# Kernel optimization log

Hardware: AMD Instinct MI355X
Metric: run time of the kernel (lower is better)

The kernel has to match this reference:

```python
import jax, jax.numpy as jnp
import numpy as np

EMBED_DIM = 2048
N_HEADS = 16
HEAD_DIM = EMBED_DIM // N_HEADS  # 128
ROPE_BASE = 10000.0


def _rope(x):
    # x: (B, H, L, d) -- torchtune-style interleaved RoPE over position axis L
    L, d = x.shape[-2], x.shape[-1]
    inv_freq = 1.0 / (ROPE_BASE ** (jnp.arange(0, d, 2, dtype=jnp.float32) / d))  # (d/2,)
    freqs = jnp.arange(L, dtype=jnp.float32)[:, None] * inv_freq[None, :]          # (L, d/2)
    cos = jnp.cos(freqs).astype(x.dtype)
    sin = jnp.sin(freqs).astype(x.dtype)
    x1 = x[..., 0::2]  # (B,H,L,d/2)
    x2 = x[..., 1::2]
    out_even = x1 * cos - x2 * sin
    out_odd = x2 * cos + x1 * sin
    return jnp.stack([out_even, out_odd], axis=-1).reshape(x.shape)


def setup_inputs() -> dict:
    key = jax.random.key(0)
    ks = jax.random.split(key, 9)
    B, L, D = 64, 256, EMBED_DIM
    x = jax.random.normal(ks[0], (B, L, D), dtype=jnp.float32)
    s = 0.02
    wq = jax.random.normal(ks[1], (D, D), dtype=jnp.float32) * s
    wk = jax.random.normal(ks[2], (D, D), dtype=jnp.float32) * s
    wv = jax.random.normal(ks[3], (D, D), dtype=jnp.float32) * s
    wo = jax.random.normal(ks[4], (D, D), dtype=jnp.float32) * s
    bq = jax.random.normal(ks[5], (D,), dtype=jnp.float32) * s
    bk = jax.random.normal(ks[6], (D,), dtype=jnp.float32) * s
    bv = jax.random.normal(ks[7], (D,), dtype=jnp.float32) * s
    bo = jax.random.normal(ks[8], (D,), dtype=jnp.float32) * s
    return {"x": x, "wq": wq, "bq": bq, "wk": wk, "bk": bk,
            "wv": wv, "bv": bv, "wo": wo, "bo": bo}


def reference(x, wq, bq, wk, bk, wv, bv, wo, bo):
    B, L, D = x.shape
    H, hd = N_HEADS, HEAD_DIM

    def proj(w, b):
        y = jnp.einsum('bld,de->ble', x, w) + b
        return y.reshape(B, L, H, hd).transpose(0, 2, 1, 3)  # (B,H,L,hd)

    q = _rope(proj(wq, bq))
    k = _rope(proj(wk, bk))
    v = proj(wv, bv)

    scale = 1.0 / jnp.sqrt(jnp.asarray(hd, dtype=x.dtype))
    scores = jnp.einsum('bhqd,bhkd->bhqk', q, k) * scale  # (B,H,L,L)
    causal = jnp.tril(jnp.ones((L, L), dtype=bool))
    scores = jnp.where(causal[None, None], scores, -jnp.inf)
    attn = jax.nn.softmax(scores, axis=-1)
    out = jnp.einsum('bhqk,bhkd->bhqd', attn, v)  # (B,H,L,hd)
    out = out.transpose(0, 2, 1, 3).reshape(B, L, D)
    return jnp.einsum('bld,de->ble', out, wo) + bo
```

## Files before the change

### kernel.cpp

```cpp
#include <hip/hip_runtime.h>
#include <math.h>

typedef __bf16 bf16;
typedef float f32x4 __attribute__((ext_vector_type(4)));
typedef bf16  bf16x4 __attribute__((ext_vector_type(4)));
typedef bf16  bf16x8 __attribute__((ext_vector_type(8)));

#define N_B  64
#define N_L  256
#define N_H  16
#define N_D  2048
#define N_HD 128
#define M_TOT (N_B * N_L)

static __device__ __forceinline__ float bfbits_lo(unsigned u) {
  union { unsigned u; float f; } c; c.u = u << 16; return c.f;
}
static __device__ __forceinline__ float bfbits_hi(unsigned u) {
  union { unsigned u; float f; } c; c.u = u & 0xffff0000u; return c.f;
}

static __device__ __forceinline__ f32x4 shflx4(f32x4 v, int m) {
  f32x4 r;
  r[0] = __shfl_xor(v[0], m);
  r[1] = __shfl_xor(v[1], m);
  r[2] = __shfl_xor(v[2], m);
  r[3] = __shfl_xor(v[3], m);
  return r;
}
static __device__ __forceinline__ f32x4 max4(f32x4 a, f32x4 b) {
  f32x4 r;
  r[0] = fmaxf(a[0], b[0]); r[1] = fmaxf(a[1], b[1]);
  r[2] = fmaxf(a[2], b[2]); r[3] = fmaxf(a[3], b[3]);
  return r;
}

__global__ void k_cast_x(const float* __restrict__ x, bf16* __restrict__ xb, int n4) {
  int i = blockIdx.x * blockDim.x + threadIdx.x;
  int st = gridDim.x * blockDim.x;
  for (; i < n4; i += st) {
    float4 v = ((const float4*)x)[i];
    bf16x4 o;
    o[0] = (bf16)v.x; o[1] = (bf16)v.y; o[2] = (bf16)v.z; o[3] = (bf16)v.w;
    ((bf16x4*)xb)[i] = o;
  }
}

__global__ void k_transpose_w(const float* __restrict__ w, bf16* __restrict__ wt) {
  __shared__ float t[32][33];
  int n0 = blockIdx.x * 32, k0 = blockIdx.y * 32;
  t[threadIdx.y][threadIdx.x] = w[(size_t)(k0 + threadIdx.y) * N_D + n0 + threadIdx.x];
  __syncthreads();
  wt[(size_t)(n0 + threadIdx.y) * N_D + k0 + threadIdx.x] = (bf16)t[threadIdx.x][threadIdx.y];
}

__global__ void k_trig(float2* __restrict__ tab) {
  int idx = blockIdx.x * blockDim.x + threadIdx.x;
  if (idx < N_L * (N_HD / 2)) {
    int l = idx >> 6, i = idx & 63;
    float ang = (float)l * powf(10000.0f, -(float)(2 * i) / 128.0f);
    tab[idx].x = cosf(ang);
    tab[idx].y = sinf(ang);
  }
}


#define GLOAD(GP, LP) __builtin_amdgcn_global_load_lds( \
    (const __attribute__((address_space(1))) void*)(GP), \
    (__attribute__((address_space(3))) void*)(LP), 16, 0, 0)
#define BARR()  __builtin_amdgcn_s_barrier()
#define SCHED() __builtin_amdgcn_sched_barrier(0)
#define PRIO1() __builtin_amdgcn_s_setprio(1)
#define PRIO0() __builtin_amdgcn_s_setprio(0)
#define WAITLGKM() asm volatile("s_waitcnt lgkmcnt(0)" ::: "memory")
#define WAITVM4()  asm volatile("s_waitcnt vmcnt(4)" ::: "memory")

#define STAGE_A(X, KT, BUF) do { \
  GLOAD(Ag + (size_t)srcOffA[0][X] + (size_t)((KT) & 31) * 64, (BUF) + ldsOffA[0][X]); \
  GLOAD(Ag + (size_t)srcOffA[1][X] + (size_t)((KT) & 31) * 64, (BUF) + ldsOffA[1][X]); \
} while (0)
#define STAGE_B(X, KT, BUF) do { \
  GLOAD(Bg + (size_t)srcOffB[0][X] + (size_t)((KT) & 31) * 64, (BUF) + ldsOffB[0][X]); \
  GLOAD(Bg + (size_t)srcOffB[1][X] + (size_t)((KT) & 31) * 64, (BUF) + ldsOffB[1][X]); \
} while (0)

#define LDA(QM, BUF) do { \
  _Pragma("unroll") for (int i_ = 0; i_ < 4; ++i_) { \
    const int R_ = wm * 128 + ((QM) * 4 + i_) * 16 + lr; \
    _Pragma("unroll") for (int kk_ = 0; kk_ < 2; ++kk_) \
      afr[i_][kk_] = *(const bf16x8*)&(BUF)[R_ * 64 + (((kk_ * 4 + lg) ^ (R_ & 7)) << 3)]; \
  } \
} while (0)
#define LDB(DST, QN, BUF) do { \
  _Pragma("unroll") for (int j_ = 0; j_ < 2; ++j_) { \
    const int R_ = wn * 64 + ((QN) * 2 + j_) * 16 + lr; \
    _Pragma("unroll") for (int kk_ = 0; kk_ < 2; ++kk_) \
      DST[j_][kk_] = *(const bf16x8*)&(BUF)[R_ * 64 + (((kk_ * 4 + lg) ^ (R_ & 7)) << 3)]; \
  } \
} while (0)

#define MFMA16(BF, QM, QN) do { \
  _Pragma("unroll") for (int i_ = 0; i_ < 4; ++i_) \
  _Pragma("unroll") for (int j_ = 0; j_ < 2; ++j_) \
  _Pragma("unroll") for (int kk_ = 0; kk_ < 2; ++kk_) \
    acc[(QM) * 4 + i_][(QN) * 2 + j_] = __builtin_amdgcn_mfma_f32_16x16x32_bf16( \
        afr[i_][kk_], BF[j_][kk_], acc[(QM) * 4 + i_][(QN) * 2 + j_], 0, 0, 0); \
} while (0)

#define TILE(T, CURA, CURB, OTHA, OTHB) do { \
   \
  LDA(0, CURA); LDB(bfr0, 0, CURB); STAGE_B(1, (T) + 1, OTHB); \
  SCHED(); BARR(); WAITLGKM(); SCHED(); \
  PRIO1(); MFMA16(bfr0, 0, 0); PRIO0(); \
  SCHED(); BARR(); SCHED(); \
   \
  LDB(bfr1, 1, CURB); STAGE_A(1, (T) + 1, OTHA); \
  SCHED(); BARR(); WAITLGKM(); SCHED(); \
  PRIO1(); MFMA16(bfr1, 0, 1); PRIO0(); \
  SCHED(); BARR(); SCHED(); \
   \
  LDA(1, CURA); STAGE_A(0, (T) + 2, CURA); \
  SCHED(); BARR(); WAITLGKM(); SCHED(); \
  PRIO1(); MFMA16(bfr0, 1, 0); PRIO0(); \
  SCHED(); BARR(); SCHED(); \
   \
  STAGE_B(0, (T) + 2, CURB); \
  SCHED(); BARR(); SCHED(); \
  PRIO1(); MFMA16(bfr1, 1, 1); PRIO0(); \
  SCHED(); WAITVM4(); BARR(); SCHED(); \
} while (0)

template<int MODE>
__global__ __launch_bounds__(512, 2) void k_gemm256(
    const bf16* __restrict__ A, const bf16* __restrict__ BT,
    const float* __restrict__ bias, void* __restrict__ dstv,
    const float2* __restrict__ tab)
{
  __shared__ bf16 lds[2][2][256 * 64];
  const int bid = blockIdx.x;
  const int xcd = bid & 7, idx = bid >> 3;
  const int bm = xcd * 8 + (idx >> 3), bn = idx & 7;
  const int m0 = bm * 256, n0 = bn * 256;
  const int tid = threadIdx.x;
  const int wave = tid >> 6, lane = tid & 63;
  const int wm = wave >> 2, wn = wave & 3;
  const int lr = lane & 15, lg = lane >> 4;
  const bf16* __restrict__ Ag = A;
  const bf16* __restrict__ Bg = BT;

  int srcOffA[2][2], srcOffB[2][2], ldsOffA[2][2], ldsOffB[2][2];
  {
    const int g7 = tid & 7;
#pragma unroll
    for (int u = 0; u < 2; ++u) {
      const int rl  = u * 64 + (tid >> 3);
      const int rl0 = u * 64 + wave * 8;
#pragma unroll
      for (int X = 0; X < 2; ++X) {
        const int rA  = ((rl >> 6) << 7)  | (X << 6) | (rl & 63);
        const int rA0 = ((rl0 >> 6) << 7) | (X << 6) | (rl0 & 63);
        srcOffA[u][X] = (m0 + rA) * N_D + ((g7 ^ (rA & 7)) << 3);
        ldsOffA[u][X] = rA0 * 64;
        const int rB  = ((rl >> 5) << 6)  | (X << 5) | (rl & 31);
        const int rB0 = ((rl0 >> 5) << 6) | (X << 5) | (rl0 & 31);
        srcOffB[u][X] = (n0 + rB) * N_D + ((g7 ^ (rB & 7)) << 3);
        ldsOffB[u][X] = rB0 * 64;
      }
    }
  }

  bf16* bufA0 = &lds[0][0][0];
  bf16* bufB0 = &lds[0][1][0];
  bf16* bufA1 = &lds[1][0][0];
  bf16* bufB1 = &lds[1][1][0];

  f32x4 acc[8][4];
#pragma unroll
  for (int i = 0; i < 8; ++i)
#pragma unroll
    for (int j = 0; j < 4; ++j)
      acc[i][j] = (f32x4){0.f, 0.f, 0.f, 0.f};

  bf16x8 afr[4][2], bfr0[2][2], bfr1[2][2];

  STAGE_A(0, 0, bufA0); STAGE_B(0, 0, bufB0);
  STAGE_B(1, 0, bufB0); STAGE_A(1, 0, bufA0);
  STAGE_A(0, 1, bufA1); STAGE_B(0, 1, bufB1);
  SCHED(); WAITVM4(); BARR(); SCHED();

#pragma unroll 1
  for (int t = 0; t < N_D / 64; t += 2) {
    TILE(t,     bufA0, bufB0, bufA1, bufB1);
    TILE(t + 1, bufA1, bufB1, bufA0, bufB0);
  }

#pragma unroll
  for (int i = 0; i < 8; ++i) {
#pragma unroll
    for (int r = 0; r < 4; ++r) {
      const int m = m0 + wm * 128 + i * 16 + lg * 4 + r;
#pragma unroll
      for (int j = 0; j < 4; ++j) {
        const int n = n0 + wn * 64 + j * 16 + lr;
        float v = acc[i][j][r] + bias[n];
        if (MODE == 3) {
          float partner = __shfl_xor(v, 1);
          const int d = n & 127, l = m & 255;
          float2 cs = tab[(l << 6) | (d >> 1)];
          v = (d & 1) ? (v * cs.x + partner * cs.y) : (v * cs.x - partner * cs.y);
        }
        if (MODE == 0 || MODE == 3) {
          bf16* dst = (bf16*)dstv;
          const int b = m >> 8, l = m & 255;
          const int h = n >> 7, d = n & 127;
          dst[(((size_t)b * N_H + h) * N_L + l) * N_HD + d] = (bf16)v;
        } else if (MODE == 2) {
          bf16* dst = (bf16*)dstv;
          const int b = m >> 8, l = m & 255;
          const int h = n >> 7, d = n & 127;
          dst[(((size_t)b * N_H + h) * N_HD + d) * N_L + l] = (bf16)v;
        } else {
          float* dst = (float*)dstv;
          dst[(size_t)m * N_D + n] = v;
        }
      }
    }
  }
}

__global__ __launch_bounds__(512) void k_attn_mfma(
    const bf16* __restrict__ Q, const bf16* __restrict__ K,
    const bf16* __restrict__ Vt, bf16* __restrict__ O)
{
  __shared__ bf16 Kl[N_L * N_HD];
  __shared__ bf16 Pl[8][16][56];

  const int bh = blockIdx.x;
  const int b = bh >> 4, h = bh & 15;
  const int tid = threadIdx.x;
  const int wave = tid >> 6, lane = tid & 63;
  const int c = lane & 15, g8 = lane >> 4;

  const bf16* Qg = Q + (size_t)bh * (N_L * N_HD);
  const bf16* Kg = K + (size_t)bh * (N_L * N_HD);
  const bf16* Vg = Vt + (size_t)bh * (N_L * N_HD);

#pragma unroll
  for (int t = 0; t < 8; ++t) {
    int idx = tid + 512 * t;
    int row = idx >> 4, g = idx & 15;
    const bf16* src = Kg + row * N_HD + ((g ^ (row & 7)) << 3);
    __builtin_amdgcn_global_load_lds(
        (const __attribute__((address_space(1))) void*)src,
        (__attribute__((address_space(3))) void*)(Kl + (size_t)wave * 512 + (size_t)t * 4096),
        16, 0, 0);
  }
  __syncthreads();

  const float scale = 0.08838834764831843f;

  for (int half = 0; half < 2; ++half) {
    const int qb = half ? (15 - wave) : wave;
    const int q0 = qb * 16;

    bf16x8 qf[4];
#pragma unroll
    for (int dk = 0; dk < 4; ++dk)
      qf[dk] = *(const bf16x8*)(Qg + (size_t)(q0 + c) * N_HD + dk * 32 + g8 * 8);

    f32x4 o[8];
#pragma unroll
    for (int dj = 0; dj < 8; ++dj) o[dj] = (f32x4){0.f, 0.f, 0.f, 0.f};
    f32x4 mrow = (f32x4){-INFINITY, -INFINITY, -INFINITY, -INFINITY};
    f32x4 lrow = (f32x4){0.f, 0.f, 0.f, 0.f};

    const int nsteps = ((q0 + 15) >> 5) + 1;
    for (int js = 0; js < nsteps; ++js) {
      const int j0 = js * 32;

      bf16x8 vf[4];
#pragma unroll
      for (int dj = 0; dj < 4; ++dj)
        vf[dj] = *(const bf16x8*)(Vg + (size_t)(dj * 16 + c) * N_L + j0 + g8 * 8);

      f32x4 s0 = (f32x4){0.f, 0.f, 0.f, 0.f};
      f32x4 s1 = (f32x4){0.f, 0.f, 0.f, 0.f};
#pragma unroll
      for (int dk = 0; dk < 4; ++dk) {
        int row0 = j0 + c;
        int row1 = j0 + 16 + c;
        bf16x8 kf0 = *(const bf16x8*)(Kl + row0 * N_HD + (((dk * 4 + g8) ^ (row0 & 7)) << 3));
        bf16x8 kf1 = *(const bf16x8*)(Kl + row1 * N_HD + (((dk * 4 + g8) ^ (row1 & 7)) << 3));
        s0 = __builtin_amdgcn_mfma_f32_16x16x32_bf16(qf[dk], kf0, s0, 0, 0, 0);
        s1 = __builtin_amdgcn_mfma_f32_16x16x32_bf16(qf[dk], kf1, s1, 0, 0, 0);
      }

      f32x4 sv0, sv1;
#pragma unroll
      for (int r = 0; r < 4; ++r) { sv0[r] = s0[r] * scale; sv1[r] = s1[r] * scale; }
      if (j0 + 31 > q0) {
#pragma unroll
        for (int r = 0; r < 4; ++r) {
          int q = q0 + g8 * 4 + r;
          if (j0 + c > q)      sv0[r] = -INFINITY;
          if (j0 + 16 + c > q) sv1[r] = -INFINITY;
        }
      }

      f32x4 mx = max4(sv0, sv1);
      mx = max4(mx, shflx4(mx, 1));
      mx = max4(mx, shflx4(mx, 2));
      mx = max4(mx, shflx4(mx, 4));
      mx = max4(mx, shflx4(mx, 8));
      f32x4 mnew = max4(mrow, mx);
      f32x4 resc, p0, p1;
#pragma unroll
      for (int r = 0; r < 4; ++r) {
        resc[r] = __expf(mrow[r] - mnew[r]);
        p0[r] = __expf(sv0[r] - mnew[r]);
        p1[r] = __expf(sv1[r] - mnew[r]);
      }
      f32x4 rsum = p0 + p1;
      rsum += shflx4(rsum, 1);
      rsum += shflx4(rsum, 2);
      rsum += shflx4(rsum, 4);
      rsum += shflx4(rsum, 8);
      lrow = lrow * resc + rsum;
      mrow = mnew;
#pragma unroll
      for (int dj = 0; dj < 8; ++dj) o[dj] *= resc;

#pragma unroll
      for (int r = 0; r < 4; ++r) {
        Pl[wave][g8 * 4 + r][c] = (bf16)p0[r];
        Pl[wave][g8 * 4 + r][16 + c] = (bf16)p1[r];
      }
      bf16x8 pf = *(const bf16x8*)&Pl[wave][c][g8 * 8];

      bf16x8 vg[4];
#pragma unroll
      for (int dj = 0; dj < 4; ++dj)
        vg[dj] = *(const bf16x8*)(Vg + (size_t)((dj + 4) * 16 + c) * N_L + j0 + g8 * 8);

#pragma unroll
      for (int dj = 0; dj < 4; ++dj)
        o[dj] = __builtin_amdgcn_mfma_f32_16x16x32_bf16(pf, vf[dj], o[dj], 0, 0, 0);
#pragma unroll
      for (int dj = 0; dj < 4; ++dj)
        o[dj + 4] = __builtin_amdgcn_mfma_f32_16x16x32_bf16(pf, vg[dj], o[dj + 4], 0, 0, 0);
    }

    f32x4 inv;
#pragma unroll
    for (int r = 0; r < 4; ++r) inv[r] = 1.0f / lrow[r];
#pragma unroll
    for (int dj = 0; dj < 8; ++dj) {
      f32x4 ov = o[dj] * inv;
#pragma unroll
      for (int r = 0; r < 4; ++r) {
        int q = q0 + g8 * 4 + r;
        int d = dj * 16 + c;
        O[(((size_t)b * N_L + q) * N_H + h) * N_HD + d] = (bf16)ov[r];
      }
    }
  }
}

extern "C" void kernel_launch(void* const* d_in, const int* in_sizes, int n_in,
                              void* d_out, int out_size, void* d_ws, size_t ws_size,
                              hipStream_t stream) {
  const float* x  = (const float*)d_in[0];
  const float* wq = (const float*)d_in[1];
  const float* bq = (const float*)d_in[2];
  const float* wk = (const float*)d_in[3];
  const float* bk = (const float*)d_in[4];
  const float* wv = (const float*)d_in[5];
  const float* bv = (const float*)d_in[6];
  const float* wo = (const float*)d_in[7];
  const float* bo = (const float*)d_in[8];

  char* ws = (char*)d_ws;
  const size_t WSZ = (size_t)N_D * N_D * sizeof(bf16);
  const size_t XSZ = (size_t)M_TOT * N_D * sizeof(bf16);
  bf16* wqT = (bf16*)(ws);
  bf16* wkT = (bf16*)(ws + WSZ);
  bf16* wvT = (bf16*)(ws + 2 * WSZ);
  bf16* woT = (bf16*)(ws + 3 * WSZ);
  bf16* xb  = (bf16*)(ws + 4 * WSZ);
  bf16* Qb  = (bf16*)(ws + 4 * WSZ + XSZ);
  bf16* Kb  = (bf16*)(ws + 4 * WSZ + 2 * XSZ);
  bf16* Vb  = (bf16*)(ws + 4 * WSZ + 3 * XSZ);
  bf16* Ob  = (bf16*)(ws + 4 * WSZ + 4 * XSZ);
  float2* tab = (float2*)(ws + 4 * WSZ + 5 * XSZ);

  k_cast_x<<<2048, 256, 0, stream>>>(x, xb, M_TOT * N_D / 4);
  dim3 tb(32, 32), tg(64, 64);
  k_transpose_w<<<tg, tb, 0, stream>>>(wq, wqT);
  k_transpose_w<<<tg, tb, 0, stream>>>(wk, wkT);
  k_transpose_w<<<tg, tb, 0, stream>>>(wv, wvT);
  k_transpose_w<<<tg, tb, 0, stream>>>(wo, woT);
  k_trig<<<64, 256, 0, stream>>>(tab);

  const int grid = (M_TOT / 256) * (N_D / 256);
  k_gemm256<3><<<grid, 512, 0, stream>>>(xb, wqT, bq, Qb, tab);
  k_gemm256<3><<<grid, 512, 0, stream>>>(xb, wkT, bk, Kb, tab);
  k_gemm256<2><<<grid, 512, 0, stream>>>(xb, wvT, bv, Vb, tab);

  k_attn_mfma<<<1024, 512, 0, stream>>>(Qb, Kb, Vb, Ob);
  k_gemm256<1><<<grid, 512, 0, stream>>>(Ob, woT, bo, d_out, tab);
}
```

Baseline: 679.6 us.

## Software-pipeline LDS fragment reads across K-halves with partial waitcnts

Restructures the GEMM inner tile so LDS fragment reads for the next K-half or M-half are issued before the current MFMA block, using double-buffered register fragments (A0b/A1b, B0b/B1b). Full lgkmcnt(0) waits and barriers are replaced by partial lgkmcnt/vmcnt waits, which lets LDS reads and global-to-LDS staging overlap with matrix math. The loop is now split by K-halves instead of N-quarters, and the first fragments are preloaded before the loop. The risks are higher register pressure at 2 waves per SIMD, and wait counts that must exactly match the outstanding loads for correctness.

```diff
diff --git a/kernel.cpp b/kernel.cpp
--- a/kernel.cpp
+++ b/kernel.cpp
@@ -72,8 +72,10 @@
 #define SCHED() __builtin_amdgcn_sched_barrier(0)
 #define PRIO1() __builtin_amdgcn_s_setprio(1)
 #define PRIO0() __builtin_amdgcn_s_setprio(0)
-#define WAITLGKM() asm volatile("s_waitcnt lgkmcnt(0)" ::: "memory")
-#define WAITVM4()  asm volatile("s_waitcnt vmcnt(4)" ::: "memory")
+#define WAITLGKM4() asm volatile("s_waitcnt lgkmcnt(4)" ::: "memory")
+#define WAITLGKM8() asm volatile("s_waitcnt lgkmcnt(8)" ::: "memory")
+#define WAITVM4()   asm volatile("s_waitcnt vmcnt(4)" ::: "memory")
+#define WAITVM6()   asm volatile("s_waitcnt vmcnt(6)" ::: "memory")
 
 #define STAGE_A(X, KT, BUF) do { \
   GLOAD(Ag + (size_t)srcOffA[0][X] + (size_t)((KT) & 31) * 64, (BUF) + ldsOffA[0][X]); \
@@ -84,50 +86,53 @@
   GLOAD(Bg + (size_t)srcOffB[1][X] + (size_t)((KT) & 31) * 64, (BUF) + ldsOffB[1][X]); \
 } while (0)
 
-#define LDA(QM, BUF) do { \
+#define RD_A(DST, MH, KK, BUF) do { \
   _Pragma("unroll") for (int i_ = 0; i_ < 4; ++i_) { \
-    const int R_ = wm * 128 + ((QM) * 4 + i_) * 16 + lr; \
-    _Pragma("unroll") for (int kk_ = 0; kk_ < 2; ++kk_) \
-      afr[i_][kk_] = *(const bf16x8*)&(BUF)[R_ * 64 + (((kk_ * 4 + lg) ^ (R_ & 7)) << 3)]; \
+    const int R_ = wm * 128 + (MH) * 64 + i_ * 16 + lr; \
+    DST[i_] = *(const bf16x8*)&(BUF)[R_ * 64 + ((((KK) * 4 + lg) ^ (R_ & 7)) << 3)]; \
   } \
 } while (0)
-#define LDB(DST, QN, BUF) do { \
-  _Pragma("unroll") for (int j_ = 0; j_ < 2; ++j_) { \
-    const int R_ = wn * 64 + ((QN) * 2 + j_) * 16 + lr; \
-    _Pragma("unroll") for (int kk_ = 0; kk_ < 2; ++kk_) \
-      DST[j_][kk_] = *(const bf16x8*)&(BUF)[R_ * 64 + (((kk_ * 4 + lg) ^ (R_ & 7)) << 3)]; \
+#define RD_B(DST, KK, BUF) do { \
+  _Pragma("unroll") for (int j_ = 0; j_ < 4; ++j_) { \
+    const int R_ = wn * 64 + j_ * 16 + lr; \
+    DST[j_] = *(const bf16x8*)&(BUF)[R_ * 64 + ((((KK) * 4 + lg) ^ (R_ & 7)) << 3)]; \
   } \
 } while (0)
 
-#define MFMA16(BF, QM, QN) do { \
+#define MFMA16(AB, BB, MH) do { \
   _Pragma("unroll") for (int i_ = 0; i_ < 4; ++i_) \
-  _Pragma("unroll") for (int j_ = 0; j_ < 2; ++j_) \
-  _Pragma("unroll") for (int kk_ = 0; kk_ < 2; ++kk_) \
-    acc[(QM) * 4 + i_][(QN) * 2 + j_] = __builtin_amdgcn_mfma_f32_16x16x32_bf16( \
-        afr[i_][kk_], BF[j_][kk_], acc[(QM) * 4 + i_][(QN) * 2 + j_], 0, 0, 0); \
+  _Pragma("unroll") for (int j_ = 0; j_ < 4; ++j_) \
+    acc[(MH) * 4 + i_][j_] = __builtin_amdgcn_mfma_f32_16x16x32_bf16( \
+        AB[i_], BB[j_], acc[(MH) * 4 + i_][j_], 0, 0, 0); \
 } while (0)
 
 #define TILE(T, CURA, CURB, OTHA, OTHB) do { \
    \
-  LDA(0, CURA); LDB(bfr0, 0, CURB); STAGE_B(1, (T) + 1, OTHB); \
-  SCHED(); BARR(); WAITLGKM(); SCHED(); \
-  PRIO1(); MFMA16(bfr0, 0, 0); PRIO0(); \
-  SCHED(); BARR(); SCHED(); \
+  STAGE_B(1, (T) + 1, OTHB); \
+  RD_A(A1b, 0, 1, CURA); RD_B(B1b, 1, CURB); \
+  SCHED(); WAITLGKM8(); SCHED(); \
+  PRIO1(); MFMA16(A0b, B0b, 0); PRIO0(); \
+  SCHED(); BARR(); \
    \
-  LDB(bfr1, 1, CURB); STAGE_A(1, (T) + 1, OTHA); \
-  SCHED(); BARR(); WAITLGKM(); SCHED(); \
-  PRIO1(); MFMA16(bfr1, 0, 1); PRIO0(); \
-  SCHED(); BARR(); SCHED(); \
+  WAITVM6(); \
+  STAGE_A(1, (T) + 1, OTHA); \
+  RD_A(A0b, 1, 0, CURA); \
+  SCHED(); WAITLGKM4(); SCHED(); \
+  PRIO1(); MFMA16(A1b, B1b, 0); PRIO0(); \
+  SCHED(); BARR(); \
    \
-  LDA(1, CURA); STAGE_A(0, (T) + 2, CURA); \
-  SCHED(); BARR(); WAITLGKM(); SCHED(); \
-  PRIO1(); MFMA16(bfr0, 1, 0); PRIO0(); \
-  SCHED(); BARR(); SCHED(); \
+  STAGE_A(0, (T) + 2, CURA); \
+  RD_A(A1b, 1, 1, CURA); \
+  SCHED(); WAITLGKM4(); SCHED(); \
+  PRIO1(); MFMA16(A0b, B0b, 1); PRIO0(); \
+  SCHED(); BARR(); \
    \
+  WAITVM4(); \
   STAGE_B(0, (T) + 2, CURB); \
-  SCHED(); BARR(); SCHED(); \
-  PRIO1(); MFMA16(bfr1, 1, 1); PRIO0(); \
-  SCHED(); WAITVM4(); BARR(); SCHED(); \
+  RD_A(A0b, 0, 0, OTHA); RD_B(B0b, 0, OTHB); \
+  SCHED(); WAITLGKM8(); SCHED(); \
+  PRIO1(); MFMA16(A1b, B1b, 1); PRIO0(); \
+  SCHED(); BARR(); \
 } while (0)
 
 template<int MODE>
@@ -181,12 +186,14 @@
     for (int j = 0; j < 4; ++j)
       acc[i][j] = (f32x4){0.f, 0.f, 0.f, 0.f};
 
-  bf16x8 afr[4][2], bfr0[2][2], bfr1[2][2];
+  bf16x8 A0b[4], A1b[4], B0b[4], B1b[4];
 
   STAGE_A(0, 0, bufA0); STAGE_B(0, 0, bufB0);
   STAGE_B(1, 0, bufB0); STAGE_A(1, 0, bufA0);
   STAGE_A(0, 1, bufA1); STAGE_B(0, 1, bufB1);
   SCHED(); WAITVM4(); BARR(); SCHED();
+  RD_A(A0b, 0, 0, bufA0); RD_B(B0b, 0, bufB0);
+  SCHED();
 
 #pragma unroll 1
   for (int t = 0; t < N_D / 64; t += 2) {
```

Result: no change. 676.1 us (-0.5%).

## Restructure GEMM to 4 waves with 128x128 per-wave tiles and register double-buffered fragments

Applied to the files above, without the earlier changes.

The 256x256 GEMM tile moves from 8 waves (128x64 per wave) to 4 waves (128x128 per wave), with launch bounds 256 threads and one block per SIMD group. LDS fragments are double-buffered in registers and LDS reads are overlapped with MFMA using partial lgkmcnt waits, and a simplified staging layout issues 8 global-to-LDS loads per operand per thread. The intent is higher arithmetic intensity per wave and fewer barriers per K-step. In exchange it raises register pressure (64 accumulator vectors plus fragments) and lowers occupancy, and the staging wait is now vmcnt(0).

```diff
diff --git a/kernel.cpp b/kernel.cpp
--- a/kernel.cpp
+++ b/kernel.cpp
@@ -72,66 +72,70 @@
 #define SCHED() __builtin_amdgcn_sched_barrier(0)
 #define PRIO1() __builtin_amdgcn_s_setprio(1)
 #define PRIO0() __builtin_amdgcn_s_setprio(0)
-#define WAITLGKM() asm volatile("s_waitcnt lgkmcnt(0)" ::: "memory")
-#define WAITVM4()  asm volatile("s_waitcnt vmcnt(4)" ::: "memory")
-
-#define STAGE_A(X, KT, BUF) do { \
-  GLOAD(Ag + (size_t)srcOffA[0][X] + (size_t)((KT) & 31) * 64, (BUF) + ldsOffA[0][X]); \
-  GLOAD(Ag + (size_t)srcOffA[1][X] + (size_t)((KT) & 31) * 64, (BUF) + ldsOffA[1][X]); \
-} while (0)
-#define STAGE_B(X, KT, BUF) do { \
-  GLOAD(Bg + (size_t)srcOffB[0][X] + (size_t)((KT) & 31) * 64, (BUF) + ldsOffB[0][X]); \
-  GLOAD(Bg + (size_t)srcOffB[1][X] + (size_t)((KT) & 31) * 64, (BUF) + ldsOffB[1][X]); \
-} while (0)
-
-#define LDA(QM, BUF) do { \
-  _Pragma("unroll") for (int i_ = 0; i_ < 4; ++i_) { \
-    const int R_ = wm * 128 + ((QM) * 4 + i_) * 16 + lr; \
-    _Pragma("unroll") for (int kk_ = 0; kk_ < 2; ++kk_) \
-      afr[i_][kk_] = *(const bf16x8*)&(BUF)[R_ * 64 + (((kk_ * 4 + lg) ^ (R_ & 7)) << 3)]; \
+#define WAITLGKM4()  asm volatile("s_waitcnt lgkmcnt(4)" ::: "memory")
+#define WAITLGKM12() asm volatile("s_waitcnt lgkmcnt(12)" ::: "memory")
+#define WAITVM4()    asm volatile("s_waitcnt vmcnt(4)" ::: "memory")
+#define WAITVM0()    asm volatile("s_waitcnt vmcnt(0)" ::: "memory")
+
+#define STAGE_A(KT, BUFA) do { \
+  _Pragma("unroll") for (int c_ = 0; c_ < 8; ++c_) \
+    GLOAD(Ag + (size_t)srcA[c_] + (size_t)((KT) & 31) * 64, (BUFA) + ldsOff[c_]); \
+} while (0)
+#define STAGE_B(KT, BUFB) do { \
+  const int bo_[8] = {0, 1, 4, 5, 2, 3, 6, 7}; \
+  _Pragma("unroll") for (int q_ = 0; q_ < 8; ++q_) { \
+    const int c_ = bo_[q_]; \
+    GLOAD(Bg + (size_t)srcB[c_] + (size_t)((KT) & 31) * 64, (BUFB) + ldsOff[c_]); \
   } \
 } while (0)
-#define LDB(DST, QN, BUF) do { \
-  _Pragma("unroll") for (int j_ = 0; j_ < 2; ++j_) { \
-    const int R_ = wn * 64 + ((QN) * 2 + j_) * 16 + lr; \
-    _Pragma("unroll") for (int kk_ = 0; kk_ < 2; ++kk_) \
-      DST[j_][kk_] = *(const bf16x8*)&(BUF)[R_ * 64 + (((kk_ * 4 + lg) ^ (R_ & 7)) << 3)]; \
+
+#define RD_A(DST, KK, BUFA) do { \
+  _Pragma("unroll") for (int i_ = 0; i_ < 8; ++i_) { \
+    const int R_ = wm * 128 + i_ * 16 + lr; \
+    DST[i_] = *(const bf16x8*)&(BUFA)[R_ * 64 + ((((KK) * 4 + lg) ^ (R_ & 7)) << 3)]; \
   } \
 } while (0)
-
-#define MFMA16(BF, QM, QN) do { \
-  _Pragma("unroll") for (int i_ = 0; i_ < 4; ++i_) \
-  _Pragma("unroll") for (int j_ = 0; j_ < 2; ++j_) \
-  _Pragma("unroll") for (int kk_ = 0; kk_ < 2; ++kk_) \
-    acc[(QM) * 4 + i_][(QN) * 2 + j_] = __builtin_amdgcn_mfma_f32_16x16x32_bf16( \
-        afr[i_][kk_], BF[j_][kk_], acc[(QM) * 4 + i_][(QN) * 2 + j_], 0, 0, 0); \
-} while (0)
-
-#define TILE(T, CURA, CURB, OTHA, OTHB) do { \
+#define RD_B(DST, NH, KK, BUFB) do { \
+  _Pragma("unroll") for (int j_ = 0; j_ < 4; ++j_) { \
+    const int R_ = wn * 128 + (NH) * 64 + j_ * 16 + lr; \
+    DST[j_] = *(const bf16x8*)&(BUFB)[R_ * 64 + ((((KK) * 4 + lg) ^ (R_ & 7)) << 3)]; \
+  } \
+} while (0)
+
+#define MFMA32(AB, BB, NH) do { \
+  _Pragma("unroll") for (int i_ = 0; i_ < 8; ++i_) \
+  _Pragma("unroll") for (int j_ = 0; j_ < 4; ++j_) \
+    acc[i_][(NH) * 4 + j_] = __builtin_amdgcn_mfma_f32_16x16x32_bf16( \
+        AB[i_], BB[j_], acc[i_][(NH) * 4 + j_], 0, 0, 0); \
+} while (0)
+
+#define TILE(T, CA, CB, OA, OB) do { \
    \
-  LDA(0, CURA); LDB(bfr0, 0, CURB); STAGE_B(1, (T) + 1, OTHB); \
-  SCHED(); BARR(); WAITLGKM(); SCHED(); \
-  PRIO1(); MFMA16(bfr0, 0, 0); PRIO0(); \
+  STAGE_A((T) + 1, OA); \
+  RD_B(B1b, 1, 0, CB); \
+  SCHED(); WAITLGKM4(); SCHED(); \
+  PRIO1(); MFMA32(A0b, B0b, 0); PRIO0(); \
   SCHED(); BARR(); SCHED(); \
    \
-  LDB(bfr1, 1, CURB); STAGE_A(1, (T) + 1, OTHA); \
-  SCHED(); BARR(); WAITLGKM(); SCHED(); \
-  PRIO1(); MFMA16(bfr1, 0, 1); PRIO0(); \
+  STAGE_B((T) + 1, OB); \
+  RD_A(A1b, 1, CA); RD_B(B0b, 0, 1, CB); \
+  SCHED(); WAITLGKM12(); SCHED(); \
+  PRIO1(); MFMA32(A0b, B1b, 1); PRIO0(); \
   SCHED(); BARR(); SCHED(); \
    \
-  LDA(1, CURA); STAGE_A(0, (T) + 2, CURA); \
-  SCHED(); BARR(); WAITLGKM(); SCHED(); \
-  PRIO1(); MFMA16(bfr0, 1, 0); PRIO0(); \
-  SCHED(); BARR(); SCHED(); \
+  RD_B(B1b, 1, 1, CB); \
+  SCHED(); WAITLGKM4(); SCHED(); \
+  PRIO1(); MFMA32(A1b, B0b, 0); PRIO0(); \
+  SCHED(); WAITVM4(); BARR(); SCHED(); \
    \
-  STAGE_B(0, (T) + 2, CURB); \
-  SCHED(); BARR(); SCHED(); \
-  PRIO1(); MFMA16(bfr1, 1, 1); PRIO0(); \
-  SCHED(); WAITVM4(); BARR(); SCHED(); \
+  RD_A(A0b, 0, OA); RD_B(B0b, 0, 0, OB); \
+  SCHED(); WAITLGKM12(); SCHED(); \
+  PRIO1(); MFMA32(A1b, B1b, 1); PRIO0(); \
+  SCHED(); WAITVM0(); BARR(); SCHED(); \
 } while (0)
 
 template<int MODE>
-__global__ __launch_bounds__(512, 2) void k_gemm256(
+__global__ __launch_bounds__(256, 1) void k_gemm256(
     const bf16* __restrict__ A, const bf16* __restrict__ BT,
     const float* __restrict__ bias, void* __restrict__ dstv,
     const float2* __restrict__ tab)
@@ -143,29 +147,20 @@
   const int m0 = bm * 256, n0 = bn * 256;
   const int tid = threadIdx.x;
   const int wave = tid >> 6, lane = tid & 63;
-  const int wm = wave >> 2, wn = wave & 3;
+  const int wm = wave >> 1, wn = wave & 1;
   const int lr = lane & 15, lg = lane >> 4;
   const bf16* __restrict__ Ag = A;
   const bf16* __restrict__ Bg = BT;
 
-  int srcOffA[2][2], srcOffB[2][2], ldsOffA[2][2], ldsOffB[2][2];
+  int srcA[8], srcB[8], ldsOff[8];
   {
-    const int g7 = tid & 7;
-#pragma unroll
-    for (int u = 0; u < 2; ++u) {
-      const int rl  = u * 64 + (tid >> 3);
-      const int rl0 = u * 64 + wave * 8;
-#pragma unroll
-      for (int X = 0; X < 2; ++X) {
-        const int rA  = ((rl >> 6) << 7)  | (X << 6) | (rl & 63);
-        const int rA0 = ((rl0 >> 6) << 7) | (X << 6) | (rl0 & 63);
-        srcOffA[u][X] = (m0 + rA) * N_D + ((g7 ^ (rA & 7)) << 3);
-        ldsOffA[u][X] = rA0 * 64;
-        const int rB  = ((rl >> 5) << 6)  | (X << 5) | (rl & 31);
-        const int rB0 = ((rl0 >> 5) << 6) | (X << 5) | (rl0 & 31);
-        srcOffB[u][X] = (n0 + rB) * N_D + ((g7 ^ (rB & 7)) << 3);
-        ldsOffB[u][X] = rB0 * 64;
-      }
+    const int g7 = tid & 7, rr = tid >> 3;
+    const int swz = (g7 ^ (rr & 7)) << 3;
+#pragma unroll
+    for (int c = 0; c < 8; ++c) {
+      srcA[c] = (m0 + c * 32 + rr) * N_D + swz;
+      srcB[c] = (n0 + c * 32 + rr) * N_D + swz;
+      ldsOff[c] = (c * 32 + wave * 8) * 64;
     }
   }
 
@@ -174,19 +169,19 @@
   bf16* bufA1 = &lds[1][0][0];
   bf16* bufB1 = &lds[1][1][0];
 
-  f32x4 acc[8][4];
+  f32x4 acc[8][8];
 #pragma unroll
   for (int i = 0; i < 8; ++i)
 #pragma unroll
-    for (int j = 0; j < 4; ++j)
+    for (int j = 0; j < 8; ++j)
       acc[i][j] = (f32x4){0.f, 0.f, 0.f, 0.f};
 
-  bf16x8 afr[4][2], bfr0[2][2], bfr1[2][2];
-
-  STAGE_A(0, 0, bufA0); STAGE_B(0, 0, bufB0);
-  STAGE_B(1, 0, bufB0); STAGE_A(1, 0, bufA0);
-  STAGE_A(0, 1, bufA1); STAGE_B(0, 1, bufB1);
-  SCHED(); WAITVM4(); BARR(); SCHED();
+  bf16x8 A0b[8], A1b[8], B0b[4], B1b[4];
+
+  STAGE_A(0, bufA0); STAGE_B(0, bufB0);
+  SCHED(); WAITVM0(); BARR(); SCHED();
+  RD_A(A0b, 0, bufA0); RD_B(B0b, 0, 0, bufB0);
+  SCHED();
 
 #pragma unroll 1
   for (int t = 0; t < N_D / 64; t += 2) {
@@ -200,8 +195,8 @@
     for (int r = 0; r < 4; ++r) {
       const int m = m0 + wm * 128 + i * 16 + lg * 4 + r;
 #pragma unroll
-      for (int j = 0; j < 4; ++j) {
-        const int n = n0 + wn * 64 + j * 16 + lr;
+      for (int j = 0; j < 8; ++j) {
+        const int n = n0 + wn * 128 + j * 16 + lr;
         float v = acc[i][j][r] + bias[n];
         if (MODE == 3) {
           float partner = __shfl_xor(v, 1);
@@ -402,10 +397,10 @@
   k_trig<<<64, 256, 0, stream>>>(tab);
 
   const int grid = (M_TOT / 256) * (N_D / 256);
-  k_gemm256<3><<<grid, 512, 0, stream>>>(xb, wqT, bq, Qb, tab);
-  k_gemm256<3><<<grid, 512, 0, stream>>>(xb, wkT, bk, Kb, tab);
-  k_gemm256<2><<<grid, 512, 0, stream>>>(xb, wvT, bv, Vb, tab);
+  k_gemm256<3><<<grid, 256, 0, stream>>>(xb, wqT, bq, Qb, tab);
+  k_gemm256<3><<<grid, 256, 0, stream>>>(xb, wkT, bk, Kb, tab);
+  k_gemm256<2><<<grid, 256, 0, stream>>>(xb, wvT, bv, Vb, tab);
 
   k_attn_mfma<<<1024, 512, 0, stream>>>(Qb, Kb, Vb, Ob);
-  k_gemm256<1><<<grid, 512, 0, stream>>>(Ob, woT, bo, d_out, tab);
-}
+  k_gemm256<1><<<grid, 256, 0, stream>>>(Ob, woT, bo, d_out, tab);
+}
```

New measurement: 2.236 ms. +229.0%, slower.
